# Optimization experiments

Measured on AMD Instinct MI355X. Metric: run time of the kernel, lower is better.

## Reference

```python
import jax, jax.numpy as jnp
import numpy as np

NUM_CHUNKS = 8
TOP_K = 2
IN_FEATURES = 4096
OUT_FEATURES = 4096
BATCH = 16384
CHUNK_IN = IN_FEATURES // NUM_CHUNKS
CHUNK_OUT = OUT_FEATURES // NUM_CHUNKS


def setup_inputs() -> dict:
    key = jax.random.key(0)
    kx, kw, kb = jax.random.split(key, 3)
    x = jax.random.normal(kx, (BATCH, IN_FEATURES), dtype=jnp.float32)
    # per-chunk expert weights, stored as [num_chunks, chunk_in, chunk_out]
    W = jax.random.normal(kw, (NUM_CHUNKS, CHUNK_IN, CHUNK_OUT), dtype=jnp.float32) * (1.0 / np.sqrt(CHUNK_IN))
    b = jax.random.normal(kb, (NUM_CHUNKS, CHUNK_OUT), dtype=jnp.float32) * 0.01
    return {"x": x, "W": W, "b": b}


def reference(x, W, b):
    B = x.shape[0]
    num_chunks, chunk_in, chunk_out = W.shape
    # torch.chunk(x, num_chunks, dim=1) == reshape to [B, num_chunks, chunk_in]
    xc = x.reshape(B, num_chunks, chunk_in)
    # per-chunk mean |x| over the whole chunk tensor (batch and features)
    activities = jnp.mean(jnp.abs(xc), axis=(0, 2))  # [num_chunks]
    _, topk_indices = jax.lax.top_k(activities, TOP_K)  # descending, like torch.topk
    # gather selected chunks and their experts, one batched matmul
    xs = xc[:, topk_indices, :]                 # [B, k, chunk_in]
    ys = jnp.einsum('bki,kio->bko', xs, W[topk_indices]) + b[topk_indices]  # [B, k, chunk_out]
    output = ys.reshape(B, TOP_K * chunk_out)   # concat along dim 1 in topk order
    return output, activities, topk_indices
```

## Files before the change

kernel.cpp:

```cpp
#include <hip/hip_runtime.h>
#include <hip/hip_bf16.h>

#define BATCH     16384
#define INFEAT    4096
#define NCHUNK    8
#define CIN       512
#define COUT      512
#define ACT_GRID  2048
#define ROWS_PER_BLOCK (BATCH / ACT_GRID)
#define OUT_MAIN  (BATCH * 1024)

typedef short bf16x8 __attribute__((ext_vector_type(8)));
typedef float f32x4  __attribute__((ext_vector_type(4)));

static __device__ inline unsigned short f2bf_rne(float f) {
    unsigned int u = __builtin_bit_cast(unsigned int, f);
    unsigned int r = (u + 0x7fffu + ((u >> 16) & 1u)) >> 16;
    return (unsigned short)r;
}

__global__ __launch_bounds__(256, 4)
void act_partial_kernel(const float* __restrict__ x, float* __restrict__ part) {
    int t = threadIdx.x;
    float acc[4] = {0.f, 0.f, 0.f, 0.f};
    int r0 = blockIdx.x * ROWS_PER_BLOCK;
    for (int r = 0; r < ROWS_PER_BLOCK; ++r) {
        const float4* p = reinterpret_cast<const float4*>(x + (size_t)(r0 + r) * INFEAT);
#pragma unroll
        for (int c = 0; c < 4; ++c) {
            float4 v = p[c * 256 + t];
            acc[c] += fabsf(v.x) + fabsf(v.y) + fabsf(v.z) + fabsf(v.w);
        }
    }
#pragma unroll
    for (int c = 0; c < 4; ++c) {
        float v = acc[c];
        v += __shfl_xor(v, 32);
        v += __shfl_xor(v, 16);
        v += __shfl_xor(v, 8);
        v += __shfl_xor(v, 4);
        v += __shfl_xor(v, 2);
        v += __shfl_xor(v, 1);
        acc[c] = v;
    }
    __shared__ float sred[16];
    int wave = t >> 6, lane = t & 63;
    if (lane == 0) {
#pragma unroll
        for (int c = 0; c < 4; ++c) sred[wave * 4 + c] = acc[c];
    }
    __syncthreads();
    if (t < 8) {
        int c = t >> 1, hi = t & 1;
        float s = sred[(2 * hi) * 4 + c] + sred[(2 * hi + 1) * 4 + c];
        part[blockIdx.x * 8 + t] = s;
    }
}

__global__ void finalize_topk_kernel(const float* __restrict__ part,
                                     float* __restrict__ out_act,
                                     float* __restrict__ out_idx,
                                     int* __restrict__ ws_idx) {
    int t = threadIdx.x;
    __shared__ double sd[256];
    __shared__ double act[8];
    int k = t & 7, s = t >> 3;
    double a = 0.0;
    for (int i = s; i < ACT_GRID; i += 32) a += (double)part[i * 8 + k];
    sd[t] = a;
    __syncthreads();
    if (t < 8) {
        double tot = 0.0;
        for (int j = 0; j < 32; ++j) tot += sd[t + 8 * j];
        double m = tot / ((double)BATCH * (double)CIN);
        act[t] = m;
        out_act[t] = (float)m;
    }
    __syncthreads();
    if (t == 0) {
        int i0 = 0;
        for (int i = 1; i < 8; ++i) if (act[i] > act[i0]) i0 = i;
        int i1 = -1;
        for (int i = 0; i < 8; ++i) {
            if (i == i0) continue;
            if (i1 < 0 || act[i] > act[i1]) i1 = i;
        }
        out_idx[0] = (float)i0;
        out_idx[1] = (float)i1;
        ws_idx[0] = i0;
        ws_idx[1] = i1;
    }
}

__global__ void wtrans_kernel(const float* __restrict__ W, const int* __restrict__ idx,
                              unsigned short* __restrict__ WT) {
    int c = blockIdx.z;
    int id = idx[c];
    __shared__ float tile[32][33];
    int tx = threadIdx.x, ty = threadIdx.y;
    const float* Wp = W + (size_t)id * (CIN * COUT);
    int i0 = blockIdx.x * 32, o0 = blockIdx.y * 32;
#pragma unroll
    for (int r = 0; r < 4; ++r)
        tile[ty + r * 8][tx] = Wp[(size_t)(i0 + ty + r * 8) * COUT + o0 + tx];
    __syncthreads();
    unsigned short* WTp = WT + (size_t)c * (CIN * COUT);
#pragma unroll
    for (int r = 0; r < 4; ++r)
        WTp[(size_t)(o0 + ty + r * 8) * CIN + i0 + tx] = f2bf_rne(tile[tx][ty + r * 8]);
}

__global__ __launch_bounds__(256, 4)
void xsel_kernel(const float* __restrict__ x, const int* __restrict__ idxp,
                 unsigned short* __restrict__ XB) {
    int c = blockIdx.y;
    int idx = idxp[c];
    size_t e0 = ((size_t)blockIdx.x * 256 + threadIdx.x) * 8;
    int r = (int)(e0 >> 9);
    int k = (int)(e0 & 511);
    const float* src = x + (size_t)r * INFEAT + idx * CIN + k;
    float4 v0 = *reinterpret_cast<const float4*>(src);
    float4 v1 = *reinterpret_cast<const float4*>(src + 4);
    ushort4 s0, s1;
    s0.x = f2bf_rne(v0.x); s0.y = f2bf_rne(v0.y); s0.z = f2bf_rne(v0.z); s0.w = f2bf_rne(v0.w);
    s1.x = f2bf_rne(v1.x); s1.y = f2bf_rne(v1.y); s1.z = f2bf_rne(v1.z); s1.w = f2bf_rne(v1.w);
    unsigned short* dst = XB + (size_t)c * (BATCH * CIN) + e0;
    *reinterpret_cast<ushort4*>(dst)     = s0;
    *reinterpret_cast<ushort4*>(dst + 4) = s1;
}

#define LDA 40
__global__ __launch_bounds__(256, 2)
void gemm_topk_kernel(const unsigned short* __restrict__ XB, const unsigned short* __restrict__ WT,
                      const float* __restrict__ bvec, const int* __restrict__ idxp,
                      float* __restrict__ out) {
    __shared__ __align__(16) unsigned short As[128 * LDA];
    __shared__ __align__(16) unsigned short Bs[128 * LDA];

    int c = blockIdx.z;
    int idx = idxp[c];
    int brow = blockIdx.x * 128;
    int bn   = blockIdx.y * 128;
    int t = threadIdx.x;
    int lane = t & 63, wid = t >> 6;
    int wm = wid >> 1, wn = wid & 1;
    int lrow = lane & 15, lgrp = lane >> 4;

    f32x4 acc[4][4] = {};

    const unsigned short* xbase = XB + (size_t)c * (BATCH * CIN) + (size_t)brow * CIN;
    const unsigned short* wtbase = WT + (size_t)c * (CIN * COUT);

    int sr = t >> 1, sh = (t & 1) * 16;

    for (int kt = 0; kt < 16; ++kt) {
        int k0 = kt * 32;
        __syncthreads();
        {
            const unsigned short* asrc = xbase + (size_t)sr * CIN + k0 + sh;
            uint4 a0 = *reinterpret_cast<const uint4*>(asrc);
            uint4 a1 = *reinterpret_cast<const uint4*>(asrc + 8);
            const unsigned short* bsrc = wtbase + (size_t)(bn + sr) * CIN + k0 + sh;
            uint4 b0 = *reinterpret_cast<const uint4*>(bsrc);
            uint4 b1 = *reinterpret_cast<const uint4*>(bsrc + 8);
            unsigned short* adst = &As[sr * LDA + sh];
            *reinterpret_cast<uint4*>(adst)     = a0;
            *reinterpret_cast<uint4*>(adst + 8) = a1;
            unsigned short* bdst = &Bs[sr * LDA + sh];
            *reinterpret_cast<uint4*>(bdst)     = b0;
            *reinterpret_cast<uint4*>(bdst + 8) = b1;
        }
        __syncthreads();
        bf16x8 af[4], bfr[4];
#pragma unroll
        for (int mi = 0; mi < 4; ++mi)
            af[mi] = *reinterpret_cast<const bf16x8*>(&As[(wm * 64 + mi * 16 + lrow) * LDA + lgrp * 8]);
#pragma unroll
        for (int ni = 0; ni < 4; ++ni)
            bfr[ni] = *reinterpret_cast<const bf16x8*>(&Bs[(wn * 64 + ni * 16 + lrow) * LDA + lgrp * 8]);
#pragma unroll
        for (int mi = 0; mi < 4; ++mi)
#pragma unroll
            for (int ni = 0; ni < 4; ++ni)
                acc[mi][ni] = __builtin_amdgcn_mfma_f32_16x16x32_bf16(af[mi], bfr[ni], acc[mi][ni], 0, 0, 0);
    }

    float bias[4];
#pragma unroll
    for (int ni = 0; ni < 4; ++ni)
        bias[ni] = bvec[idx * COUT + bn + wn * 64 + ni * 16 + lrow];
#pragma unroll
    for (int mi = 0; mi < 4; ++mi) {
#pragma unroll
        for (int r = 0; r < 4; ++r) {
            int row = brow + wm * 64 + mi * 16 + lgrp * 4 + r;
            float* orow = out + (size_t)row * 1024 + c * 512 + bn + wn * 64;
#pragma unroll
            for (int ni = 0; ni < 4; ++ni)
                orow[ni * 16 + lrow] = acc[mi][ni][r] + bias[ni];
        }
    }
}

extern "C" void kernel_launch(void* const* d_in, const int* in_sizes, int n_in,
                              void* d_out, int out_size, void* d_ws, size_t ws_size,
                              hipStream_t stream) {
    const float* x = (const float*)d_in[0];
    const float* W = (const float*)d_in[1];
    const float* b = (const float*)d_in[2];
    float* out = (float*)d_out;

    float* part = (float*)d_ws;
    int* ws_idx = (int*)((char*)d_ws + 65536);
    unsigned short* WT = (unsigned short*)((char*)d_ws + 65792);
    unsigned short* XB = (unsigned short*)((char*)d_ws + 65792 + 2 * CIN * COUT * 2);

    act_partial_kernel<<<ACT_GRID, 256, 0, stream>>>(x, part);
    finalize_topk_kernel<<<1, 256, 0, stream>>>(part, out + OUT_MAIN, out + OUT_MAIN + 8, ws_idx);
    wtrans_kernel<<<dim3(16, 16, 2), dim3(32, 8), 0, stream>>>(W, ws_idx, WT);
    xsel_kernel<<<dim3(BATCH * CIN / (256 * 8), 2), 256, 0, stream>>>(x, ws_idx, XB);
    gemm_topk_kernel<<<dim3(BATCH / 128, COUT / 128, 2), 256, 0, stream>>>(XB, WT, b, ws_idx, out);
}
```

Before: 127.8 us.

## Use direct global-to-LDS loads with XOR swizzle and larger K tile in GEMM

The GEMM now stages A and B tiles with global_load_lds 16-byte copies straight into shared memory, skipping the register round trip. The K tile grows from 32 to 64 with an XOR-swizzled layout in place of padding, to avoid bank conflicts on the fragment reads. Launch bounds move to 4 blocks per CU. The aim is fewer instructions and fewer barriers per K step in the main matmul. The swizzle must match exactly between writer and reader, and the higher occupancy target may squeeze registers.

Result: no change. 130.3 us (+2.0%).

```diff
diff --git a/kernel.cpp b/kernel.cpp
--- a/kernel.cpp
+++ b/kernel.cpp
@@ -17,6 +17,12 @@
     unsigned int u = __builtin_bit_cast(unsigned int, f);
     unsigned int r = (u + 0x7fffu + ((u >> 16) & 1u)) >> 16;
     return (unsigned short)r;
+}
+
+static __device__ inline void gload16(const void* g, void* l) {
+    __builtin_amdgcn_global_load_lds(
+        (const __attribute__((address_space(1))) unsigned int*)g,
+        (__attribute__((address_space(3))) unsigned int*)l, 16, 0, 0);
 }
 
 __global__ __launch_bounds__(256, 4)
@@ -129,13 +135,13 @@
     *reinterpret_cast<ushort4*>(dst + 4) = s1;
 }
 
-#define LDA 40
-__global__ __launch_bounds__(256, 2)
+#define GBK 64
+__global__ __launch_bounds__(256, 4)
 void gemm_topk_kernel(const unsigned short* __restrict__ XB, const unsigned short* __restrict__ WT,
                       const float* __restrict__ bvec, const int* __restrict__ idxp,
                       float* __restrict__ out) {
-    __shared__ __align__(16) unsigned short As[128 * LDA];
-    __shared__ __align__(16) unsigned short Bs[128 * LDA];
+    __shared__ __align__(16) unsigned short As[128 * GBK];
+    __shared__ __align__(16) unsigned short Bs[128 * GBK];
 
     int c = blockIdx.z;
     int idx = idxp[c];
@@ -148,41 +154,43 @@
 
     f32x4 acc[4][4] = {};
 
-    const unsigned short* xbase = XB + (size_t)c * (BATCH * CIN) + (size_t)brow * CIN;
-    const unsigned short* wtbase = WT + (size_t)c * (CIN * COUT);
-
-    int sr = t >> 1, sh = (t & 1) * 16;
-
-    for (int kt = 0; kt < 16; ++kt) {
-        int k0 = kt * 32;
+    int srow = wid * 32 + (lane >> 3);
+    int swz  = ((lane & 7) ^ (lane >> 3)) * 8;
+    const unsigned short* agp = XB + (size_t)c * (BATCH * CIN) + (size_t)(brow + srow) * CIN + swz;
+    const unsigned short* bgp = WT + (size_t)c * (CIN * COUT) + (size_t)(bn + srow) * CIN + swz;
+    char* aldst = (char*)As + (size_t)(wid * 32) * (GBK * 2);
+    char* bldst = (char*)Bs + (size_t)(wid * 32) * (GBK * 2);
+
+    for (int kt = 0; kt < CIN / GBK; ++kt) {
+        int k0 = kt * GBK;
         __syncthreads();
-        {
-            const unsigned short* asrc = xbase + (size_t)sr * CIN + k0 + sh;
-            uint4 a0 = *reinterpret_cast<const uint4*>(asrc);
-            uint4 a1 = *reinterpret_cast<const uint4*>(asrc + 8);
-            const unsigned short* bsrc = wtbase + (size_t)(bn + sr) * CIN + k0 + sh;
-            uint4 b0 = *reinterpret_cast<const uint4*>(bsrc);
-            uint4 b1 = *reinterpret_cast<const uint4*>(bsrc + 8);
-            unsigned short* adst = &As[sr * LDA + sh];
-            *reinterpret_cast<uint4*>(adst)     = a0;
-            *reinterpret_cast<uint4*>(adst + 8) = a1;
-            unsigned short* bdst = &Bs[sr * LDA + sh];
-            *reinterpret_cast<uint4*>(bdst)     = b0;
-            *reinterpret_cast<uint4*>(bdst + 8) = b1;
+#pragma unroll
+        for (int j = 0; j < 4; ++j) {
+            gload16(agp + (size_t)j * 8 * CIN + k0, aldst + j * 8 * (GBK * 2));
+            gload16(bgp + (size_t)j * 8 * CIN + k0, bldst + j * 8 * (GBK * 2));
         }
         __syncthreads();
-        bf16x8 af[4], bfr[4];
-#pragma unroll
-        for (int mi = 0; mi < 4; ++mi)
-            af[mi] = *reinterpret_cast<const bf16x8*>(&As[(wm * 64 + mi * 16 + lrow) * LDA + lgrp * 8]);
-#pragma unroll
-        for (int ni = 0; ni < 4; ++ni)
-            bfr[ni] = *reinterpret_cast<const bf16x8*>(&Bs[(wn * 64 + ni * 16 + lrow) * LDA + lgrp * 8]);
-#pragma unroll
-        for (int mi = 0; mi < 4; ++mi)
-#pragma unroll
-            for (int ni = 0; ni < 4; ++ni)
-                acc[mi][ni] = __builtin_amdgcn_mfma_f32_16x16x32_bf16(af[mi], bfr[ni], acc[mi][ni], 0, 0, 0);
+#pragma unroll
+        for (int kk = 0; kk < 2; ++kk) {
+            bf16x8 af[4], bfr[4];
+#pragma unroll
+            for (int mi = 0; mi < 4; ++mi) {
+                int row = wm * 64 + mi * 16 + lrow;
+                af[mi] = *reinterpret_cast<const bf16x8*>(
+                    &As[row * GBK + (((kk * 4 + lgrp) ^ (lrow & 7)) * 8)]);
+            }
+#pragma unroll
+            for (int ni = 0; ni < 4; ++ni) {
+                int row = wn * 64 + ni * 16 + lrow;
+                bfr[ni] = *reinterpret_cast<const bf16x8*>(
+                    &Bs[row * GBK + (((kk * 4 + lgrp) ^ (lrow & 7)) * 8)]);
+            }
+#pragma unroll
+            for (int mi = 0; mi < 4; ++mi)
+#pragma unroll
+                for (int ni = 0; ni < 4; ++ni)
+                    acc[mi][ni] = __builtin_amdgcn_mfma_f32_16x16x32_bf16(af[mi], bfr[ni], acc[mi][ni], 0, 0, 0);
+        }
     }
 
     float bias[4];
```
